# Performance work log

Hardware: AMD Instinct MI355X
Metric: run time of the kernel (lower is better)

Reference implementation:

```python
import jax, jax.numpy as jnp
import numpy as np

B, PH = 1, 4
D, H, W = 48, 256, 256          # target volume size (module init `size`)
DM, HM, WM = 48, 128, 128       # MVF stored at (1, 1/2, 1/2) resolution; resized by (1,2,2)


def setup_inputs() -> dict:
    key = jax.random.key(0)
    k1, k2 = jax.random.split(key)
    # complex image passed as real/imag pair (torch.view_as_real layout)
    image = jax.random.normal(k1, (B, 1, D, H, W, 2), dtype=jnp.float32)
    # motion vector field: [b, ph, 3, d, h/2, w/2], displacements in voxel units
    mvf_kernels = jax.random.normal(k2, (B, PH, 3, DM, HM, WM), dtype=jnp.float32)
    return {"image": image, "mvf_kernels": mvf_kernels}


def _grid_sample_3d(vol, coords):
    """Trilinear grid-sample, zeros padding, align_corners=True semantics.

    vol:    [N, C, D, H, W]
    coords: [N, 3, D, H, W] absolute voxel coordinates, channel order (z, y, x).
    Matches VoxelMorph SpatialTransformNetwork: new_locs = grid + flow, then
    F.grid_sample(..., mode='bilinear', align_corners=True) whose normalization
    round-trips exactly back to voxel coordinates.
    """
    N, C, Dv, Hv, Wv = vol.shape
    z, y, x = coords[:, 0], coords[:, 1], coords[:, 2]
    z0 = jnp.floor(z); y0 = jnp.floor(y); x0 = jnp.floor(x)
    wz = z - z0; wy = y - y0; wx = x - x0
    z0i = z0.astype(jnp.int32); y0i = y0.astype(jnp.int32); x0i = x0.astype(jnp.int32)
    vol_flat = vol.reshape(N, C, Dv * Hv * Wv)

    def corner(zi, yi, xi, w):
        valid = ((zi >= 0) & (zi < Dv) & (yi >= 0) & (yi < Hv)
                 & (xi >= 0) & (xi < Wv))
        zc = jnp.clip(zi, 0, Dv - 1)
        yc = jnp.clip(yi, 0, Hv - 1)
        xc = jnp.clip(xi, 0, Wv - 1)
        idx = (zc * Hv + yc) * Wv + xc                              # [N,D,H,W]
        vals = jax.vmap(lambda vf, ix: vf[:, ix])(vol_flat, idx)    # [N,C,D,H,W]
        return vals * (w * valid.astype(vol.dtype))[:, None]

    out = corner(z0i,     y0i,     x0i,     (1 - wz) * (1 - wy) * (1 - wx))
    out = out + corner(z0i,     y0i,     x0i + 1, (1 - wz) * (1 - wy) * wx)
    out = out + corner(z0i,     y0i + 1, x0i,     (1 - wz) * wy * (1 - wx))
    out = out + corner(z0i,     y0i + 1, x0i + 1, (1 - wz) * wy * wx)
    out = out + corner(z0i + 1, y0i,     x0i,     wz * (1 - wy) * (1 - wx))
    out = out + corner(z0i + 1, y0i,     x0i + 1, wz * (1 - wy) * wx)
    out = out + corner(z0i + 1, y0i + 1, x0i,     wz * wy * (1 - wx))
    out = out + corner(z0i + 1, y0i + 1, x0i + 1, wz * wy * wx)
    return out


def reference(image, mvf_kernels):
    b, ph = mvf_kernels.shape[0], mvf_kernels.shape[1]
    dt = mvf_kernels.dtype

    # generate_forward_operator: rearrange + resize_deformation_field(_, (1,2,2))
    mvf = mvf_kernels.reshape(b * ph, 3, DM, HM, WM)
    mvf = jax.image.resize(mvf, (b * ph, 3, D, H, W), method='trilinear')
    # deformation magnitudes scale with the spatial resize factors (1,2,2)
    mvf = mvf * jnp.array([1.0, 2.0, 2.0], dt).reshape(1, 3, 1, 1, 1)

    # 'b () d h w comp -> (b ph) comp d h w' (broadcast over ph)
    img = jnp.moveaxis(image[:, 0], -1, 1)          # [b, 2, D, H, W]
    image_move = jnp.repeat(img, ph, axis=0)        # [(b ph), 2, D, H, W]

    grid = jnp.stack(
        jnp.meshgrid(jnp.arange(D, dtype=dt), jnp.arange(H, dtype=dt),
                     jnp.arange(W, dtype=dt), indexing='ij'), axis=0)  # [3,D,H,W]
    coords = grid[None] + mvf                       # [(b ph), 3, D, H, W]

    warped = _grid_sample_3d(image_move, coords)    # [(b ph), 2, D, H, W]

    # '(b ph) comp d h w -> b ph d h w comp'
    image_4ph = jnp.moveaxis(warped.reshape(b, ph, 2, D, H, W), 2, -1)

    # torch.cat((image, image_4ph), dim=1); trailing axis = (real, imag)
    return jnp.concatenate([image, image_4ph], axis=1)  # [b, 1+ph, D, H, W, 2]
```

## Files before the change

### kernel.cpp

```cpp
#include <hip/hip_runtime.h>

#define DD 48
#define HH 256
#define WW 256
#define HM 128
#define WM 128
#define PLANE (DD*HH*WW)
#define MPLANE (DD*HM*WM)

#define SZ 13
#define SY 27
#define SXL 27
#define SLICE (SY*SXL)
#define SCELLS (SZ*SLICE)

typedef __attribute__((ext_vector_type(2))) float f32x2;

#define MVF_PAIR(da, db, vo, bp) \
  asm volatile("global_load_dwordx2 %0, %2, %3\n\t" \
               "global_load_dwordx2 %1, %2, %3 offset:512" \
               : "=&v"(da), "=&v"(db) : "v"(vo), "s"(bp))

#define GLD(d, p) \
  asm volatile("global_load_dwordx2 %0, %1, off" : "=&v"(d) : "v"(p))

#define DSR(d, a, offstr) \
  asm volatile("ds_read_b64 %0, %1 offset:" offstr : "=v"(d) : "v"(a))

__global__ __launch_bounds__(512, 4) void mvf_warp(
    const float* __restrict__ img,
    const float* __restrict__ mvf,
    float* __restrict__ out)
{
    extern __shared__ f32x2 S[];
    const f32x2* img2 = (const f32x2*)img;
    f32x2* out2 = (f32x2*)out;
    const int tid = threadIdx.x;

    const int bid = blockIdx.x;
    const int xcd = bid & 7;
    const int lin = bid >> 3;
    const int tx  = lin & 15;
    const int rest = lin >> 4;
    const int ty  = xcd * 2 + (rest & 1);
    const int tz  = rest >> 1;

    const int z0t = tz * 8, y0t = ty * 16, x0t = tx * 16;
    const int oz = z0t - 2, oy = y0t - 5, ox = x0t - 5;

    const int x  = x0t + (tid & 15);
    const int y  = y0t + ((tid >> 4) & 15);
    const int zb = z0t + (tid >> 8);

    float ys = fminf(fmaxf((float)y * 0.5f - 0.25f, 0.0f), 127.0f);
    float xs = fminf(fmaxf((float)x * 0.5f - 0.25f, 0.0f), 127.0f);
    int my0 = min((int)ys, HM - 2);
    int mx0 = min((int)xs, WM - 2);
    float wyk = ys - (float)my0, wxk = xs - (float)mx0;
    float w00 = (1.0f - wyk) * (1.0f - wxk);
    float w01 = (1.0f - wyk) * wxk;
    float w10 = wyk * (1.0f - wxk);
    float w11 = wyk * wxk;

    const unsigned voff0 = (unsigned)((zb * (HM*WM) + my0 * WM + mx0) * 4);

    f32x2 Ra[2][6], Rb[2][6];

    MVF_PAIR(Ra[0][0], Rb[0][0], voff0, mvf + 0*MPLANE);
    MVF_PAIR(Ra[0][1], Rb[0][1], voff0, mvf + 1*MPLANE);
    MVF_PAIR(Ra[0][2], Rb[0][2], voff0, mvf + 2*MPLANE);
    MVF_PAIR(Ra[0][3], Rb[0][3], voff0, mvf + 3*MPLANE);
    MVF_PAIR(Ra[0][4], Rb[0][4], voff0, mvf + 4*MPLANE);
    MVF_PAIR(Ra[0][5], Rb[0][5], voff0, mvf + 5*MPLANE);
    __builtin_amdgcn_sched_barrier(0);

    {
        int c0 = tid;
        int iy0 = c0 / SXL, ix0 = c0 - iy0 * SXL;
        int gy0 = oy + iy0, gx0 = ox + ix0;
        bool vy0 = (gy0 >= 0) && (gy0 < HH) && (gx0 >= 0) && (gx0 < WW);
        int yx0 = min(max(gy0,0),HH-1) * WW + min(max(gx0,0),WW-1);
        int c1 = tid + 512;
        int iy1 = c1 / SXL, ix1 = c1 - iy1 * SXL;
        int gy1 = oy + iy1, gx1 = ox + ix1;
        bool vy1 = (gy1 >= 0) && (gy1 < HH) && (gx1 >= 0) && (gx1 < WW);
        int yx1 = min(max(gy1,0),HH-1) * WW + min(max(gx1,0),WW-1);
        bool has2 = (c1 < SLICE);

        f32x2 ga[SZ], gbv[SZ];
#pragma unroll
        for (int iz = 0; iz < SZ; ++iz) {
            int gz = oz + iz;
            int gb = min(max(gz,0),DD-1) * (HH*WW);
            GLD(ga[iz], img2 + gb + yx0);
        }
        if (has2) {
#pragma unroll
            for (int iz = 0; iz < SZ; ++iz) {
                int gz = oz + iz;
                int gb = min(max(gz,0),DD-1) * (HH*WW);
                GLD(gbv[iz], img2 + gb + yx1);
            }
        }
        __builtin_amdgcn_sched_barrier(0);
        asm volatile("s_waitcnt vmcnt(0)" ::: "memory");
        __builtin_amdgcn_sched_barrier(0);
#pragma unroll
        for (int iz = 0; iz < SZ; ++iz) {
            int gz = oz + iz;
            bool vz = (gz >= 0) && (gz < DD);
            f32x2 v0 = ga[iz];
            if (!(vz && vy0)) { v0.x = 0.0f; v0.y = 0.0f; }
            S[iz*SLICE + c0] = v0;
        }
        if (has2) {
#pragma unroll
            for (int iz = 0; iz < SZ; ++iz) {
                int gz = oz + iz;
                bool vz = (gz >= 0) && (gz < DD);
                f32x2 v1 = gbv[iz];
                if (!(vz && vy1)) { v1.x = 0.0f; v1.y = 0.0f; }
                S[iz*SLICE + c1] = v1;
            }
        }
    }
    __syncthreads();

    const int obase = (zb*HH + y)*WW + x;
    const int lzb = zb - oz;
    const int lyc = y - oy;
    const int lxc = x - ox;

#pragma unroll
    for (int k = 0; k < 4; ++k)
        out2[obase + k*(2*HH*WW)] = S[((lzb + 2*k)*SY + lyc)*SXL + lxc];

    unsigned fm = 0;

#pragma unroll
    for (int hb = 0; hb < 8; ++hb) {
        const int k = hb >> 1;
        const int h = hb & 1;
        const int r = hb & 1;

        if (hb < 7) {
            const int kn = (hb + 1) >> 1;
            const int rn = (hb + 1) & 1;
            const int cb = ((hb + 1) & 1) * 6;
            unsigned vo = voff0 + (unsigned)(kn * 131072);
            MVF_PAIR(Ra[rn][0], Rb[rn][0], vo, mvf + (cb+0)*MPLANE);
            MVF_PAIR(Ra[rn][1], Rb[rn][1], vo, mvf + (cb+1)*MPLANE);
            MVF_PAIR(Ra[rn][2], Rb[rn][2], vo, mvf + (cb+2)*MPLANE);
            MVF_PAIR(Ra[rn][3], Rb[rn][3], vo, mvf + (cb+3)*MPLANE);
            MVF_PAIR(Ra[rn][4], Rb[rn][4], vo, mvf + (cb+4)*MPLANE);
            MVF_PAIR(Ra[rn][5], Rb[rn][5], vo, mvf + (cb+5)*MPLANE);
            asm volatile("s_waitcnt vmcnt(12)" ::: "memory");
        } else {
            asm volatile("s_waitcnt vmcnt(0)" ::: "memory");
        }
        __builtin_amdgcn_sched_barrier(0);

        float mvzA = w00*Ra[r][0].x + w01*Ra[r][0].y + w10*Rb[r][0].x + w11*Rb[r][0].y;
        float mvyA = w00*Ra[r][1].x + w01*Ra[r][1].y + w10*Rb[r][1].x + w11*Rb[r][1].y;
        float mvxA = w00*Ra[r][2].x + w01*Ra[r][2].y + w10*Rb[r][2].x + w11*Rb[r][2].y;
        float mvzB = w00*Ra[r][3].x + w01*Ra[r][3].y + w10*Rb[r][3].x + w11*Rb[r][3].y;
        float mvyB = w00*Ra[r][4].x + w01*Ra[r][4].y + w10*Rb[r][4].x + w11*Rb[r][4].y;
        float mvxB = w00*Ra[r][5].x + w01*Ra[r][5].y + w10*Rb[r][5].x + w11*Rb[r][5].y;

        float tzA = (float)(lzb + 2*k) + mvzA;
        float tyA = (float)lyc + 2.0f*mvyA;
        float txA = (float)lxc + 2.0f*mvxA;
        float fzA = floorf(tzA), fyA = floorf(tyA), fxA = floorf(txA);
        int lzA = (int)fzA, lyA = (int)fyA, lxA = (int)fxA;
        float wzA = tzA - fzA, wyA = tyA - fyA, wxA = txA - fxA;
        bool okA = ((unsigned)lzA <= SZ-2) && ((unsigned)lyA <= SY-2) &&
                   ((unsigned)lxA <= SXL-2);
        unsigned baseA = okA ? (unsigned)(((lzA*SY + lyA)*SXL + lxA)*8) : 0u;

        float tzB = (float)(lzb + 2*k) + mvzB;
        float tyB = (float)lyc + 2.0f*mvyB;
        float txB = (float)lxc + 2.0f*mvxB;
        float fzB = floorf(tzB), fyB = floorf(tyB), fxB = floorf(txB);
        int lzB = (int)fzB, lyB = (int)fyB, lxB = (int)fxB;
        float wzB = tzB - fzB, wyB = tyB - fyB, wxB = txB - fxB;
        bool okB = ((unsigned)lzB <= SZ-2) && ((unsigned)lyB <= SY-2) &&
                   ((unsigned)lxB <= SXL-2);
        unsigned baseB = okB ? (unsigned)(((lzB*SY + lyB)*SXL + lxB)*8) : 0u;

        fm |= (okA ? 0u : 1u) << (hb*2 + 0);
        fm |= (okB ? 0u : 1u) << (hb*2 + 1);

        f32x2 qa[8], qb[8];
        DSR(qa[0], baseA, "0");    DSR(qa[1], baseA, "8");
        DSR(qa[2], baseA, "216");  DSR(qa[3], baseA, "224");
        DSR(qa[4], baseA, "5832"); DSR(qa[5], baseA, "5840");
        DSR(qa[6], baseA, "6048"); DSR(qa[7], baseA, "6056");
        DSR(qb[0], baseB, "0");    DSR(qb[1], baseB, "8");
        DSR(qb[2], baseB, "216");  DSR(qb[3], baseB, "224");
        DSR(qb[4], baseB, "5832"); DSR(qb[5], baseB, "5840");
        DSR(qb[6], baseB, "6048"); DSR(qb[7], baseB, "6056");

        asm volatile("s_waitcnt lgkmcnt(0)" ::: "memory");
        __builtin_amdgcn_sched_barrier(0);
        {
            float e0x = qa[0].x + wxA*(qa[1].x - qa[0].x);
            float e0y = qa[0].y + wxA*(qa[1].y - qa[0].y);
            float e1x = qa[2].x + wxA*(qa[3].x - qa[2].x);
            float e1y = qa[2].y + wxA*(qa[3].y - qa[2].y);
            float e2x = qa[4].x + wxA*(qa[5].x - qa[4].x);
            float e2y = qa[4].y + wxA*(qa[5].y - qa[4].y);
            float e3x = qa[6].x + wxA*(qa[7].x - qa[6].x);
            float e3y = qa[6].y + wxA*(qa[7].y - qa[6].y);
            float g0x = e0x + wyA*(e1x - e0x);
            float g0y = e0y + wyA*(e1y - e0y);
            float g1x = e2x + wyA*(e3x - e2x);
            float g1y = e2y + wyA*(e3y - e2y);
            f32x2 res;
            res.x = g0x + wzA*(g1x - g0x);
            res.y = g0y + wzA*(g1y - g0y);
            if (okA) out2[(2*h + 1)*PLANE + k*(2*HH*WW) + obase] = res;
        }
        {
            float e0x = qb[0].x + wxB*(qb[1].x - qb[0].x);
            float e0y = qb[0].y + wxB*(qb[1].y - qb[0].y);
            float e1x = qb[2].x + wxB*(qb[3].x - qb[2].x);
            float e1y = qb[2].y + wxB*(qb[3].y - qb[2].y);
            float e2x = qb[4].x + wxB*(qb[5].x - qb[4].x);
            float e2y = qb[4].y + wxB*(qb[5].y - qb[4].y);
            float e3x = qb[6].x + wxB*(qb[7].x - qb[6].x);
            float e3y = qb[6].y + wxB*(qb[7].y - qb[6].y);
            float g0x = e0x + wyB*(e1x - e0x);
            float g0y = e0y + wyB*(e1y - e0y);
            float g1x = e2x + wyB*(e3x - e2x);
            float g1y = e2y + wyB*(e3y - e2y);
            f32x2 res;
            res.x = g0x + wzB*(g1x - g0x);
            res.y = g0y + wzB*(g1y - g0y);
            if (okB) out2[(2*h + 2)*PLANE + k*(2*HH*WW) + obase] = res;
        }
    }

    asm volatile("s_waitcnt vmcnt(0) lgkmcnt(0)" ::: "memory");
#pragma unroll 1
    for (int s = 0; s < 16; ++s) {
        if (fm & (1u << s)) {
            int k = s >> 2, p = s & 3;
            int z = zb + 2*k;
            const float* mp = mvf + (z*(HM*WM) + my0*WM + mx0);
            float mv[3];
#pragma unroll
            for (int ch = 0; ch < 3; ++ch) {
                const float* m = mp + (p*3 + ch)*MPLANE;
                float2 a = *(const float2*)m;
                float2 b = *(const float2*)(m + WM);
                mv[ch] = w00*a.x + w01*a.y + w10*b.x + w11*b.y;
            }
            float zc = (float)z + mv[0];
            float yc = (float)y + 2.0f*mv[1];
            float xc = (float)x + 2.0f*mv[2];
            float zf = floorf(zc), yf = floorf(yc), xf = floorf(xc);
            int zi = (int)zf, yi = (int)yf, xi = (int)xf;
            float wz = zc - zf, wy2 = yc - yf, wx2 = xc - xf;
            int zc0 = min(max(zi,0),DD-1), zc1 = min(max(zi+1,0),DD-1);
            int yc0 = min(max(yi,0),HH-1), yc1 = min(max(yi+1,0),HH-1);
            int xb  = min(max(xi,0),WW-2);
            float s0 = (zi >= 0  && zi < DD)     ? (1.0f - wz)  : 0.0f;
            float s1 = (zi >= -1 && zi < DD - 1) ? wz           : 0.0f;
            float t0 = (yi >= 0  && yi < HH)     ? (1.0f - wy2) : 0.0f;
            float t1 = (yi >= -1 && yi < HH - 1) ? wy2          : 0.0f;
            int d = xi - xb;
            float u0 = (d == 0) ? (1.0f - wx2) : ((d == -1) ? wx2 : 0.0f);
            float u1 = (d == 0) ? wx2 : ((d == 1) ? (1.0f - wx2) : 0.0f);
            int g00 = (zc0*HH + yc0)*WW + xb;
            int g01 = (zc0*HH + yc1)*WW + xb;
            int g10 = (zc1*HH + yc0)*WW + xb;
            int g11 = (zc1*HH + yc1)*WW + xb;
            f32x2 p00L = img2[g00], p00H = img2[g00 + 1];
            f32x2 p01L = img2[g01], p01H = img2[g01 + 1];
            f32x2 p10L = img2[g10], p10H = img2[g10 + 1];
            f32x2 p11L = img2[g11], p11H = img2[g11 + 1];
            float r0a = u0*p00L.x + u1*p00H.x, r0b = u0*p00L.y + u1*p00H.y;
            float r1a = u0*p01L.x + u1*p01H.x, r1b = u0*p01L.y + u1*p01H.y;
            float r2a = u0*p10L.x + u1*p10H.x, r2b = u0*p10L.y + u1*p10H.y;
            float r3a = u0*p11L.x + u1*p11H.x, r3b = u0*p11L.y + u1*p11H.y;
            f32x2 res;
            res.x = s0*(t0*r0a + t1*r1a) + s1*(t0*r2a + t1*r3a);
            res.y = s0*(t0*r0b + t1*r1b) + s1*(t0*r2b + t1*r3b);
            out2[(p + 1)*PLANE + (z*HH + y)*WW + x] = res;
        }
    }
}

extern "C" void kernel_launch(void* const* d_in, const int* in_sizes, int n_in,
                              void* d_out, int out_size, void* d_ws, size_t ws_size,
                              hipStream_t stream) {
    const float* img = (const float*)d_in[0];
    const float* mvf = (const float*)d_in[1];
    float* out = (float*)d_out;

    mvf_warp<<<1536, 512, SCELLS * sizeof(f32x2), stream>>>(img, mvf, out);
}
```

Before: 59.03 us.

## Deepen MVF prefetch to three buffers and pair LDS corner reads with ds_read2_b64

The MVF register ring grows from two stages to three. The second stage's loads are issued before the barrier, and each iteration prefetches two half-steps ahead with looser vmcnt waits, so global latency has more time to hide behind LDS and compute work. The eight ds_read_b64 corner fetches per sample collapse into four ds_read2_b64 instructions, using 8-byte-unit offsets and a separate base for the z+1 slice, which cuts LDS instruction count. The cost is another 24 VGPRs for the extra MVF stage under launch_bounds(512,4), which risks spills or lower occupancy.

```diff
diff --git a/kernel.cpp b/kernel.cpp
--- a/kernel.cpp
+++ b/kernel.cpp
@@ -15,6 +15,7 @@
 #define SCELLS (SZ*SLICE)
 
 typedef __attribute__((ext_vector_type(2))) float f32x2;
+typedef __attribute__((ext_vector_type(4))) float f32x4;
 
 #define MVF_PAIR(da, db, vo, bp) \
   asm volatile("global_load_dwordx2 %0, %2, %3\n\t" \
@@ -24,8 +25,9 @@
 #define GLD(d, p) \
   asm volatile("global_load_dwordx2 %0, %1, off" : "=&v"(d) : "v"(p))
 
-#define DSR(d, a, offstr) \
-  asm volatile("ds_read_b64 %0, %1 offset:" offstr : "=v"(d) : "v"(a))
+#define DSR2(d, a, o0, o1) \
+  asm volatile("ds_read2_b64 %0, %1 offset0:" o0 " offset1:" o1 \
+               : "=v"(d) : "v"(a))
 
 __global__ __launch_bounds__(512, 4) void mvf_warp(
     const float* __restrict__ img,
@@ -64,7 +66,7 @@
 
     const unsigned voff0 = (unsigned)((zb * (HM*WM) + my0 * WM + mx0) * 4);
 
-    f32x2 Ra[2][6], Rb[2][6];
+    f32x2 Ra[3][6], Rb[3][6];
 
     MVF_PAIR(Ra[0][0], Rb[0][0], voff0, mvf + 0*MPLANE);
     MVF_PAIR(Ra[0][1], Rb[0][1], voff0, mvf + 1*MPLANE);
@@ -124,6 +126,14 @@
             }
         }
     }
+
+    MVF_PAIR(Ra[1][0], Rb[1][0], voff0, mvf + 6*MPLANE);
+    MVF_PAIR(Ra[1][1], Rb[1][1], voff0, mvf + 7*MPLANE);
+    MVF_PAIR(Ra[1][2], Rb[1][2], voff0, mvf + 8*MPLANE);
+    MVF_PAIR(Ra[1][3], Rb[1][3], voff0, mvf + 9*MPLANE);
+    MVF_PAIR(Ra[1][4], Rb[1][4], voff0, mvf + 10*MPLANE);
+    MVF_PAIR(Ra[1][5], Rb[1][5], voff0, mvf + 11*MPLANE);
+    __builtin_amdgcn_sched_barrier(0);
     __syncthreads();
 
     const int obase = (zb*HH + y)*WW + x;
@@ -141,19 +151,21 @@
     for (int hb = 0; hb < 8; ++hb) {
         const int k = hb >> 1;
         const int h = hb & 1;
-        const int r = hb & 1;
-
-        if (hb < 7) {
-            const int kn = (hb + 1) >> 1;
-            const int rn = (hb + 1) & 1;
-            const int cb = ((hb + 1) & 1) * 6;
-            unsigned vo = voff0 + (unsigned)(kn * 131072);
+        const int r = hb % 3;
+
+        if (hb < 6) {
+            const int hbn = hb + 2;
+            const int rn = hbn % 3;
+            const int cb = (hbn & 1) * 6;
+            unsigned vo = voff0 + (unsigned)((hbn >> 1) * 131072);
             MVF_PAIR(Ra[rn][0], Rb[rn][0], vo, mvf + (cb+0)*MPLANE);
             MVF_PAIR(Ra[rn][1], Rb[rn][1], vo, mvf + (cb+1)*MPLANE);
             MVF_PAIR(Ra[rn][2], Rb[rn][2], vo, mvf + (cb+2)*MPLANE);
             MVF_PAIR(Ra[rn][3], Rb[rn][3], vo, mvf + (cb+3)*MPLANE);
             MVF_PAIR(Ra[rn][4], Rb[rn][4], vo, mvf + (cb+4)*MPLANE);
             MVF_PAIR(Ra[rn][5], Rb[rn][5], vo, mvf + (cb+5)*MPLANE);
+            asm volatile("s_waitcnt vmcnt(24)" ::: "memory");
+        } else if (hb == 6) {
             asm volatile("s_waitcnt vmcnt(12)" ::: "memory");
         } else {
             asm volatile("s_waitcnt vmcnt(0)" ::: "memory");
@@ -190,27 +202,30 @@
         fm |= (okA ? 0u : 1u) << (hb*2 + 0);
         fm |= (okB ? 0u : 1u) << (hb*2 + 1);
 
-        f32x2 qa[8], qb[8];
-        DSR(qa[0], baseA, "0");    DSR(qa[1], baseA, "8");
-        DSR(qa[2], baseA, "216");  DSR(qa[3], baseA, "224");
-        DSR(qa[4], baseA, "5832"); DSR(qa[5], baseA, "5840");
-        DSR(qa[6], baseA, "6048"); DSR(qa[7], baseA, "6056");
-        DSR(qb[0], baseB, "0");    DSR(qb[1], baseB, "8");
-        DSR(qb[2], baseB, "216");  DSR(qb[3], baseB, "224");
-        DSR(qb[4], baseB, "5832"); DSR(qb[5], baseB, "5840");
-        DSR(qb[6], baseB, "6048"); DSR(qb[7], baseB, "6056");
+        unsigned baseZA = baseA + 5832u;
+        unsigned baseZB = baseB + 5832u;
+
+        f32x4 pa01, pa23, pa45, pa67, pb01, pb23, pb45, pb67;
+        DSR2(pa01, baseA,  "0",  "1");
+        DSR2(pa23, baseA,  "27", "28");
+        DSR2(pa45, baseZA, "0",  "1");
+        DSR2(pa67, baseZA, "27", "28");
+        DSR2(pb01, baseB,  "0",  "1");
+        DSR2(pb23, baseB,  "27", "28");
+        DSR2(pb45, baseZB, "0",  "1");
+        DSR2(pb67, baseZB, "27", "28");
 
         asm volatile("s_waitcnt lgkmcnt(0)" ::: "memory");
         __builtin_amdgcn_sched_barrier(0);
         {
-            float e0x = qa[0].x + wxA*(qa[1].x - qa[0].x);
-            float e0y = qa[0].y + wxA*(qa[1].y - qa[0].y);
-            float e1x = qa[2].x + wxA*(qa[3].x - qa[2].x);
-            float e1y = qa[2].y + wxA*(qa[3].y - qa[2].y);
-            float e2x = qa[4].x + wxA*(qa[5].x - qa[4].x);
-            float e2y = qa[4].y + wxA*(qa[5].y - qa[4].y);
-            float e3x = qa[6].x + wxA*(qa[7].x - qa[6].x);
-            float e3y = qa[6].y + wxA*(qa[7].y - qa[6].y);
+            float e0x = pa01.x + wxA*(pa01.z - pa01.x);
+            float e0y = pa01.y + wxA*(pa01.w - pa01.y);
+            float e1x = pa23.x + wxA*(pa23.z - pa23.x);
+            float e1y = pa23.y + wxA*(pa23.w - pa23.y);
+            float e2x = pa45.x + wxA*(pa45.z - pa45.x);
+            float e2y = pa45.y + wxA*(pa45.w - pa45.y);
+            float e3x = pa67.x + wxA*(pa67.z - pa67.x);
+            float e3y = pa67.y + wxA*(pa67.w - pa67.y);
             float g0x = e0x + wyA*(e1x - e0x);
             float g0y = e0y + wyA*(e1y - e0y);
             float g1x = e2x + wyA*(e3x - e2x);
@@ -221,14 +236,14 @@
             if (okA) out2[(2*h + 1)*PLANE + k*(2*HH*WW) + obase] = res;
         }
         {
-            float e0x = qb[0].x + wxB*(qb[1].x - qb[0].x);
-            float e0y = qb[0].y + wxB*(qb[1].y - qb[0].y);
-            float e1x = qb[2].x + wxB*(qb[3].x - qb[2].x);
-            float e1y = qb[2].y + wxB*(qb[3].y - qb[2].y);
-            float e2x = qb[4].x + wxB*(qb[5].x - qb[4].x);
-            float e2y = qb[4].y + wxB*(qb[5].y - qb[4].y);
-            float e3x = qb[6].x + wxB*(qb[7].x - qb[6].x);
-            float e3y = qb[6].y + wxB*(qb[7].y - qb[6].y);
+            float e0x = pb01.x + wxB*(pb01.z - pb01.x);
+            float e0y = pb01.y + wxB*(pb01.w - pb01.y);
+            float e1x = pb23.x + wxB*(pb23.z - pb23.x);
+            float e1y = pb23.y + wxB*(pb23.w - pb23.y);
+            float e2x = pb45.x + wxB*(pb45.z - pb45.x);
+            float e2y = pb45.y + wxB*(pb45.w - pb45.y);
+            float e3x = pb67.x + wxB*(pb67.z - pb67.x);
+            float e3y = pb67.y + wxB*(pb67.w - pb67.y);
             float g0x = e0x + wyB*(e1x - e0x);
             float g0y = e0y + wyB*(e1y - e0y);
             float g1x = e2x + wyB*(e3x - e2x);
```

Result: no change. 58.04 us, median of 2 (-1.7%).
